# Optimization experiments

Hardware: AMD Instinct MI355X
Metric: run time of the kernel (lower is better)

## Reference

```python
import jax, jax.numpy as jnp
import numpy as np

H, W = 16, 16
DIM = 512
HEADS = 8
DIM_HEAD = 64
INNER = HEADS * DIM_HEAD  # 512
B = 8
N = H * W  # 256
SCALE = DIM_HEAD ** -0.5
EPS = 1e-5


def _index_map(h, w):
    # index_map[n, m] = dx * (2w-1) + dy with dx = x-i+h-1, dy = y-j+w-1
    xs = np.arange(h)
    ys = np.arange(w)
    dx = xs[:, None] - xs[None, :] + h - 1            # (h, h)
    dy = ys[:, None] - ys[None, :] + w - 1            # (w, w)
    idx = dx[:, None, :, None] * (2 * w - 1) + dy[None, :, None, :]  # (h, w, h, w)
    return idx.reshape(h * w, h * w).astype(np.int32)


def setup_inputs() -> dict:
    key = jax.random.key(0)
    ks = jax.random.split(key, 5)
    x = jax.random.normal(ks[0], (B, N, DIM), dtype=jnp.float32)
    ln_g = jnp.ones((DIM,), jnp.float32)
    ln_b = jnp.zeros((DIM,), jnp.float32)
    w_qkv = jax.random.normal(ks[1], (DIM, 3 * INNER), jnp.float32) * 0.02
    unique_params = jax.random.normal(ks[2], ((2 * H - 1) * (2 * W - 1), INNER), jnp.float32) * 0.02
    w_out = jax.random.normal(ks[3], (INNER, DIM), jnp.float32) * 0.02
    b_out = jnp.zeros((DIM,), jnp.float32)
    idx_map = jnp.asarray(_index_map(H, W))  # (N, N) int32
    return {"x": x, "ln_g": ln_g, "ln_b": ln_b, "w_qkv": w_qkv,
            "unique_params": unique_params, "w_out": w_out, "b_out": b_out,
            "idx_map": idx_map}


def reference(x, ln_g, ln_b, w_qkv, unique_params, w_out, b_out, idx_map):
    b, n, _ = x.shape
    # LayerNorm
    mu = jnp.mean(x, axis=-1, keepdims=True)
    var = jnp.mean(jnp.square(x - mu), axis=-1, keepdims=True)
    xn = (x - mu) * jax.lax.rsqrt(var + EPS) * ln_g + ln_b
    # qkv projection (no bias)
    qkv = xn @ w_qkv                                  # (b, n, 3*inner)
    q, k, v = jnp.split(qkv, 3, axis=-1)
    q = q.reshape(b, n, HEADS, DIM_HEAD)
    k = k.reshape(b, n, HEADS, DIM_HEAD)
    v = v.reshape(b, n, HEADS, DIM_HEAD)
    # attention scores
    dots = jnp.einsum('bnhd,bmhd->bhnm', q, k) * SCALE
    attn = jax.nn.softmax(dots, axis=-1)              # (b, h, n, m)
    # relative-position table: (n, m, h, d)
    rpos = unique_params[idx_map].reshape(n, n, HEADS, DIM_HEAD)
    # out[b,h,n,d] = sum_m attn[b,h,n,m] * (v[b,m,h,d] + rpos[n,m,h,d])
    out = jnp.einsum('bhnm,bmhd->bnhd', attn, v) \
        + jnp.einsum('bhnm,nmhd->bnhd', attn, rpos)
    out = out.reshape(b, n, INNER)
    return out @ w_out + b_out
```

## Files before the change

kernel.cpp:

```cpp
#include <hip/hip_runtime.h>
#include <math.h>

#define NB 8
#define SEQ 256
#define DIMC 512
#define NHEAD 8
#define DHEAD 64
#define SCALEF 0.125f

typedef __attribute__((ext_vector_type(8))) short s16x8;
typedef __attribute__((ext_vector_type(4))) float f32x4;

typedef __attribute__((address_space(3))) unsigned int lds_u32_t;
typedef const __attribute__((address_space(1))) unsigned int g_u32_t;
static __device__ __forceinline__ void gl_lds16(const void* gsrc, void* ldst) {
  __builtin_amdgcn_global_load_lds((g_u32_t*)gsrc, (lds_u32_t*)ldst, 16, 0, 0);
}

static __device__ __forceinline__ unsigned short f2bf(float f) {
  union { float f; unsigned u; } c; c.f = f;
  unsigned r = c.u + 0x7FFF + ((c.u >> 16) & 1);
  return (unsigned short)(r >> 16);
}

static __device__ void tcast_body(const float* __restrict__ W,
    unsigned short* __restrict__ WT, int K, int N, int n0, int k0, int t,
    float (*tile)[65]) {
#pragma unroll
  for (int i = 0; i < 16; ++i) {
    const int idx = i * 256 + t;
    const int kl = idx >> 6, nl = idx & 63;
    tile[kl][nl] = W[(size_t)(k0 + kl) * N + n0 + nl];
  }
  __syncthreads();
#pragma unroll
  for (int i = 0; i < 16; ++i) {
    const int idx = i * 256 + t;
    const int nl = idx >> 6, kl = idx & 63;
    WT[(size_t)(n0 + nl) * K + k0 + kl] = f2bf(tile[kl][nl]);
  }
}

__global__ __launch_bounds__(256) void prep_kernel(const float* __restrict__ x,
    const float* __restrict__ g, const float* __restrict__ bta,
    const float* __restrict__ w_qkv, const float* __restrict__ w_out,
    const float* __restrict__ up, unsigned short* __restrict__ xnb,
    unsigned short* __restrict__ wqt, unsigned short* __restrict__ wot,
    unsigned short* __restrict__ upT) {
  __shared__ float tile[64][65];
  __shared__ float sh_s[4], sh_q[4];
  const int t = threadIdx.x;
  const int bid = blockIdx.x;
  if (bid < 192) {
    tcast_body(w_qkv, wqt, 512, 1536, (bid % 24) * 64, (bid / 24) * 64, t, tile);
  } else if (bid < 256) {
    const int b2 = bid - 192;
    tcast_body(w_out, wot, 512, 512, (b2 % 8) * 64, (b2 / 8) * 64, t, tile);
  } else if (bid < 384) {
    const int b2 = bid - 256;
    const int k0 = (b2 >> 3) * 64, n0 = (b2 & 7) * 64;
#pragma unroll
    for (int i = 0; i < 16; ++i) {
      const int idx = i * 256 + t;
      const int kl = idx >> 6, nl = idx & 63;
      const int k = k0 + kl;
      tile[kl][nl] = (k < 961) ? up[(size_t)k * 512 + n0 + nl] : 0.0f;
    }
    __syncthreads();
#pragma unroll
    for (int i = 0; i < 16; ++i) {
      const int idx = i * 256 + t;
      const int nl = idx >> 6, kl = idx & 63;
      if (k0 + kl < 992)
        upT[(size_t)(n0 + nl) * 992 + k0 + kl] = f2bf(tile[kl][nl]);
    }
  } else {
    const int row = bid - 384;
    const float2 v = ((const float2*)(x + (size_t)row * DIMC))[t];
    float s = v.x + v.y;
    float q = v.x * v.x + v.y * v.y;
#pragma unroll
    for (int off = 32; off > 0; off >>= 1) {
      s += __shfl_down(s, off);
      q += __shfl_down(q, off);
    }
    const int wave = t >> 6, lane = t & 63;
    if (lane == 0) { sh_s[wave] = s; sh_q[wave] = q; }
    __syncthreads();
    const float fs = sh_s[0] + sh_s[1] + sh_s[2] + sh_s[3];
    const float fq = sh_q[0] + sh_q[1] + sh_q[2] + sh_q[3];
    const float mean = fs * (1.0f / DIMC);
    const float inv = rsqrtf(fq * (1.0f / DIMC) - mean * mean + 1e-5f);
    const float2 gv = ((const float2*)g)[t];
    const float2 bv = ((const float2*)bta)[t];
    ushort2 o;
    o.x = f2bf((v.x - mean) * inv * gv.x + bv.x);
    o.y = f2bf((v.y - mean) * inv * gv.y + bv.y);
    ((ushort2*)(xnb + (size_t)row * DIMC))[t] = o;
  }
}

template <int BM, int BN, bool BIAS, bool OUTBF, bool VSPLIT>
__global__ __launch_bounds__(256) void mfma_gemm_bt(
    const unsigned short* __restrict__ A, const unsigned short* __restrict__ BT,
    const float* __restrict__ bias, void* __restrict__ Cv,
    unsigned short* __restrict__ vtb, int M, int K, int N) {
  constexpr int TR = BM / 32;
  constexpr int TC = BN / 32;
  __shared__ unsigned short As[BM * 32];
  __shared__ unsigned short Bs[BN * 32];
  const int t = threadIdx.x;
  const int wave = t >> 6, lane = t & 63;
  const int wr = wave >> 1, wc = wave & 1;
  const int bm = blockIdx.x * BM, bn = blockIdx.y * BN;

  f32x4 acc[TR][TC] = {};

  const int fr = lane & 15, q4 = lane >> 4;
  const int kBlocks = K >> 5;
  for (int kb = 0; kb < kBlocks; ++kb) {
    const int k0 = kb << 5;
    __syncthreads();
#pragma unroll
    for (int c = 0; c < (BM * 4 + 255) / 256; ++c) {
      const int p = c * 256 + t;
      if (BM * 4 % 256 == 0 || p < BM * 4) {
        const int row = p >> 2;
        const int jl = (p & 3) ^ ((row >> 1) & 3);
        gl_lds16(A + (size_t)(bm + row) * K + k0 + jl * 8,
                 As + (size_t)(c * 256 + wave * 64) * 8);
      }
    }
#pragma unroll
    for (int c = 0; c < (BN * 4 + 255) / 256; ++c) {
      const int p = c * 256 + t;
      if (BN * 4 % 256 == 0 || p < BN * 4) {
        const int row = p >> 2;
        const int jl = (p & 3) ^ ((row >> 1) & 3);
        gl_lds16(BT + (size_t)(bn + row) * K + k0 + jl * 8,
                 Bs + (size_t)(c * 256 + wave * 64) * 8);
      }
    }
    __syncthreads();
    s16x8 af[TR], bfr[TC];
#pragma unroll
    for (int i = 0; i < TR; ++i) {
      const int row = wr * (BM / 2) + i * 16 + fr;
      const int jp = q4 ^ ((row >> 1) & 3);
      af[i] = *(const s16x8*)(As + row * 32 + jp * 8);
    }
#pragma unroll
    for (int j = 0; j < TC; ++j) {
      const int row = wc * (BN / 2) + j * 16 + fr;
      const int jp = q4 ^ ((row >> 1) & 3);
      bfr[j] = *(const s16x8*)(Bs + row * 32 + jp * 8);
    }
#pragma unroll
    for (int i = 0; i < TR; ++i)
#pragma unroll
      for (int j = 0; j < TC; ++j)
        acc[i][j] = __builtin_amdgcn_mfma_f32_16x16x32_bf16(af[i], bfr[j],
                                                            acc[i][j], 0, 0, 0);
  }
  if (VSPLIT && bn >= 1024) {
#pragma unroll
    for (int i = 0; i < TR; ++i) {
#pragma unroll
      for (int j = 0; j < TC; ++j) {
        const int hc = bn - 1024 + wc * (BN / 2) + j * 16 + fr;
        const int h = hc >> 6, d = hc & 63;
#pragma unroll
        for (int r = 0; r < 4; ++r) {
          const int row = bm + wr * (BM / 2) + i * 16 + q4 * 4 + r;
          const int b = row >> 8, m = row & 255;
          vtb[(size_t)((b * 8 + h) * 64 + d) * 256 + m] = f2bf(acc[i][j][r]);
        }
      }
    }
    return;
  }
#pragma unroll
  for (int i = 0; i < TR; ++i) {
#pragma unroll
    for (int j = 0; j < TC; ++j) {
      const int col = bn + wc * (BN / 2) + j * 16 + fr;
      const float bv = BIAS ? bias[col] : 0.0f;
#pragma unroll
      for (int r = 0; r < 4; ++r) {
        const int row = bm + wr * (BM / 2) + i * 16 + q4 * 4 + r;
        if constexpr (OUTBF) {
          ((unsigned short*)Cv)[(size_t)row * N + col] = f2bf(acc[i][j][r] + bv);
        } else {
          ((float*)Cv)[(size_t)row * N + col] = acc[i][j][r] + bv;
        }
      }
    }
  }
}

#define PSTR 264
#define ASTR2 520
__global__ __launch_bounds__(256) void attn_rpos_kernel(
    const unsigned short* __restrict__ qkvb,
    const unsigned short* __restrict__ vtb,
    const unsigned short* __restrict__ upT,
    unsigned short* __restrict__ ob) {
  __shared__ unsigned short ascat[16 * ASTR2];
  __shared__ unsigned short p_lds[16 * PSTR];
  __shared__ float smax[4][16], ssum[4][16];
  const int bh = blockIdx.y, b = bh >> 3, h = bh & 7;
  const int xn = blockIdx.x;
  const int n0 = xn * 16;
  const int t = threadIdx.x, wave = t >> 6, lane = t & 63;
  const int fr = lane & 15, q4 = lane >> 4;
  const int kwin0 = (xn * 31) & ~7;

  {
    const s16x8 z = {0, 0, 0, 0, 0, 0, 0, 0};
#pragma unroll
    for (int i = 0; i < 5; ++i) {
      const int idx = i * 256 + t;
      if (idx < 16 * ASTR2 / 8) *(s16x8*)(ascat + idx * 8) = z;
    }
  }

  s16x8 qf[2];
  {
    const size_t qrow = (size_t)(b * SEQ + n0 + fr) * 1536 + h * 64;
#pragma unroll
    for (int ks = 0; ks < 2; ++ks)
      qf[ks] = *(const s16x8*)(qkvb + qrow + ks * 32 + q4 * 8);
  }

  f32x4 s[4];
#pragma unroll
  for (int j = 0; j < 4; ++j) s[j] = (f32x4){0.f, 0.f, 0.f, 0.f};
  {
    const unsigned short* kb =
        qkvb + (size_t)(b * SEQ + wave * 64 + fr) * 1536 + 512 + h * 64;
#pragma unroll
    for (int ks = 0; ks < 2; ++ks)
#pragma unroll
      for (int j = 0; j < 4; ++j) {
        const s16x8 kf =
            *(const s16x8*)(kb + (size_t)j * (16 * 1536) + ks * 32 + q4 * 8);
        s[j] = __builtin_amdgcn_mfma_f32_16x16x32_bf16(qf[ks], kf, s[j], 0, 0, 0);
      }
  }

  float mx[4] = {-1e30f, -1e30f, -1e30f, -1e30f};
#pragma unroll
  for (int j = 0; j < 4; ++j)
#pragma unroll
    for (int r = 0; r < 4; ++r) {
      s[j][r] *= SCALEF;
      mx[r] = fmaxf(mx[r], s[j][r]);
    }
#pragma unroll
  for (int r = 0; r < 4; ++r) {
    mx[r] = fmaxf(mx[r], __shfl_xor(mx[r], 1));
    mx[r] = fmaxf(mx[r], __shfl_xor(mx[r], 2));
    mx[r] = fmaxf(mx[r], __shfl_xor(mx[r], 4));
    mx[r] = fmaxf(mx[r], __shfl_xor(mx[r], 8));
  }
  if (fr == 0) {
#pragma unroll
    for (int r = 0; r < 4; ++r) smax[wave][q4 * 4 + r] = mx[r];
  }
  __syncthreads();

  float fm[4];
#pragma unroll
  for (int r = 0; r < 4; ++r) {
    const int row = q4 * 4 + r;
    fm[r] = fmaxf(fmaxf(smax[0][row], smax[1][row]),
                  fmaxf(smax[2][row], smax[3][row]));
  }
  float sum[4] = {0.f, 0.f, 0.f, 0.f};
#pragma unroll
  for (int j = 0; j < 4; ++j)
#pragma unroll
    for (int r = 0; r < 4; ++r) {
      s[j][r] = __expf(s[j][r] - fm[r]);
      sum[r] += s[j][r];
    }
#pragma unroll
  for (int r = 0; r < 4; ++r) {
    sum[r] += __shfl_xor(sum[r], 1);
    sum[r] += __shfl_xor(sum[r], 2);
    sum[r] += __shfl_xor(sum[r], 4);
    sum[r] += __shfl_xor(sum[r], 8);
  }
  if (fr == 0) {
#pragma unroll
    for (int r = 0; r < 4; ++r) ssum[wave][q4 * 4 + r] = sum[r];
  }
  __syncthreads();

  float invs[4];
#pragma unroll
  for (int r = 0; r < 4; ++r) {
    const int row = q4 * 4 + r;
    invs[r] = 1.0f / (ssum[0][row] + ssum[1][row] + ssum[2][row] + ssum[3][row]);
  }

#pragma unroll
  for (int j = 0; j < 4; ++j) {
    const int mt = wave * 4 + j;
#pragma unroll
    for (int r = 0; r < 4; ++r) {
      const int row = q4 * 4 + r;
      const unsigned short pb = f2bf(s[j][r] * invs[r]);
      p_lds[row * PSTR + mt * 16 + fr] = pb;
      const int c = (xn - mt + 15) * 31 + (row - fr + 15) - kwin0;
      ascat[row * ASTR2 + c] = pb;
    }
  }
  __syncthreads();

  f32x4 oA = (f32x4){0.f, 0.f, 0.f, 0.f}, oB = oA, oC = oA, oD = oA;
  {
    const unsigned short* uB =
        upT + (size_t)(h * 64 + wave * 16 + fr) * 992 + kwin0;
    const unsigned short* aR = ascat + fr * ASTR2;
#pragma unroll
    for (int ks = 0; ks < 8; ++ks) {
      const s16x8 af = *(const s16x8*)(aR + ks * 32 + q4 * 8);
      const s16x8 bfg = *(const s16x8*)(uB + ks * 32 + q4 * 8);
      oA = __builtin_amdgcn_mfma_f32_16x16x32_bf16(af, bfg, oA, 0, 0, 0);
    }
#pragma unroll
    for (int ks = 8; ks < 16; ++ks) {
      const s16x8 af = *(const s16x8*)(aR + ks * 32 + q4 * 8);
      const s16x8 bfg = *(const s16x8*)(uB + ks * 32 + q4 * 8);
      oB = __builtin_amdgcn_mfma_f32_16x16x32_bf16(af, bfg, oB, 0, 0, 0);
    }
  }
  {
    const unsigned short* vB = vtb + (size_t)(bh * 64 + wave * 16 + fr) * 256;
    const unsigned short* pR = p_lds + fr * PSTR;
#pragma unroll
    for (int ks = 0; ks < 4; ++ks) {
      const s16x8 pf = *(const s16x8*)(pR + ks * 32 + q4 * 8);
      const s16x8 vfg = *(const s16x8*)(vB + ks * 32 + q4 * 8);
      oC = __builtin_amdgcn_mfma_f32_16x16x32_bf16(pf, vfg, oC, 0, 0, 0);
    }
#pragma unroll
    for (int ks = 4; ks < 8; ++ks) {
      const s16x8 pf = *(const s16x8*)(pR + ks * 32 + q4 * 8);
      const s16x8 vfg = *(const s16x8*)(vB + ks * 32 + q4 * 8);
      oD = __builtin_amdgcn_mfma_f32_16x16x32_bf16(pf, vfg, oD, 0, 0, 0);
    }
  }
  const f32x4 o = (oA + oB) + (oC + oD);
#pragma unroll
  for (int r = 0; r < 4; ++r) {
    const int n = n0 + q4 * 4 + r;
    ob[(size_t)(b * SEQ + n) * DIMC + h * 64 + wave * 16 + fr] = f2bf(o[r]);
  }
}

extern "C" void kernel_launch(void* const* d_in, const int* in_sizes, int n_in,
                              void* d_out, int out_size, void* d_ws,
                              size_t ws_size, hipStream_t stream) {
  const float* x = (const float*)d_in[0];
  const float* ln_g = (const float*)d_in[1];
  const float* ln_b = (const float*)d_in[2];
  const float* w_qkv = (const float*)d_in[3];
  const float* up = (const float*)d_in[4];
  const float* w_out = (const float*)d_in[5];
  const float* b_out = (const float*)d_in[6];
  float* out = (float*)d_out;

  unsigned short* u = (unsigned short*)d_ws;
  unsigned short* qkvb = u;
  unsigned short* xnb = u + 3145728;
  unsigned short* ob = u + 4194304;
  unsigned short* wqt = u + 5242880;
  unsigned short* wot = u + 6029312;
  unsigned short* upT = u + 6291456;
  unsigned short* vtb = u + 6799360;
  if (ws_size < (size_t)7847936 * sizeof(unsigned short)) return;

  prep_kernel<<<2432, 256, 0, stream>>>(x, ln_g, ln_b, w_qkv, w_out, up,
                                        xnb, wqt, wot, upT);
  mfma_gemm_bt<64, 64, false, true, true>
      <<<dim3(32, 24), 256, 0, stream>>>(xnb, wqt, nullptr, qkvb, vtb,
                                         2048, 512, 1536);
  attn_rpos_kernel<<<dim3(16, 64), 256, 0, stream>>>(qkvb, vtb, upT, ob);
  mfma_gemm_bt<64, 32, true, false, false>
      <<<dim3(32, 16), 256, 0, stream>>>(ob, wot, b_out, out, nullptr,
                                         2048, 512, 512);
}
```

Measured before the change: 111.3 us.

## Load GEMM fragments directly from global memory and add MFMA priority hints

The two projection GEMMs no longer stage A and B tiles through LDS with global_load_lds and barriers. Each wave now loads its MFMA fragments straight from global memory, with K fixed at compile time and the loop unrolled by four. The V-transpose epilogue packs four bf16 values into a single ushort4 store, and the attention kernel wraps its MFMA loops in s_setprio. This removes LDS traffic and block barriers, at the cost of redundant global and L2 reads across waves plus strided, less coalesced fragment loads.

```diff
diff --git a/kernel.cpp b/kernel.cpp
--- a/kernel.cpp
+++ b/kernel.cpp
@@ -1,21 +1,12 @@
 #include <hip/hip_runtime.h>
 #include <math.h>
 
-#define NB 8
 #define SEQ 256
 #define DIMC 512
-#define NHEAD 8
-#define DHEAD 64
 #define SCALEF 0.125f
 
 typedef __attribute__((ext_vector_type(8))) short s16x8;
 typedef __attribute__((ext_vector_type(4))) float f32x4;
-
-typedef __attribute__((address_space(3))) unsigned int lds_u32_t;
-typedef const __attribute__((address_space(1))) unsigned int g_u32_t;
-static __device__ __forceinline__ void gl_lds16(const void* gsrc, void* ldst) {
-  __builtin_amdgcn_global_load_lds((g_u32_t*)gsrc, (lds_u32_t*)ldst, 16, 0, 0);
-}
 
 static __device__ __forceinline__ unsigned short f2bf(float f) {
   union { float f; unsigned u; } c; c.f = f;
@@ -100,61 +91,32 @@
   }
 }
 
-template <int BM, int BN, bool BIAS, bool OUTBF, bool VSPLIT>
-__global__ __launch_bounds__(256) void mfma_gemm_bt(
+template <int BM, int BN, int K, bool BIAS, bool OUTBF, bool VSPLIT>
+__global__ __launch_bounds__(256) void gemm_direct(
     const unsigned short* __restrict__ A, const unsigned short* __restrict__ BT,
     const float* __restrict__ bias, void* __restrict__ Cv,
-    unsigned short* __restrict__ vtb, int M, int K, int N) {
+    unsigned short* __restrict__ vtb, int M, int N) {
   constexpr int TR = BM / 32;
   constexpr int TC = BN / 32;
-  __shared__ unsigned short As[BM * 32];
-  __shared__ unsigned short Bs[BN * 32];
   const int t = threadIdx.x;
   const int wave = t >> 6, lane = t & 63;
   const int wr = wave >> 1, wc = wave & 1;
+  const int fr = lane & 15, q4 = lane >> 4;
   const int bm = blockIdx.x * BM, bn = blockIdx.y * BN;
 
   f32x4 acc[TR][TC] = {};
-
-  const int fr = lane & 15, q4 = lane >> 4;
-  const int kBlocks = K >> 5;
-  for (int kb = 0; kb < kBlocks; ++kb) {
-    const int k0 = kb << 5;
-    __syncthreads();
-#pragma unroll
-    for (int c = 0; c < (BM * 4 + 255) / 256; ++c) {
-      const int p = c * 256 + t;
-      if (BM * 4 % 256 == 0 || p < BM * 4) {
-        const int row = p >> 2;
-        const int jl = (p & 3) ^ ((row >> 1) & 3);
-        gl_lds16(A + (size_t)(bm + row) * K + k0 + jl * 8,
-                 As + (size_t)(c * 256 + wave * 64) * 8);
-      }
-    }
-#pragma unroll
-    for (int c = 0; c < (BN * 4 + 255) / 256; ++c) {
-      const int p = c * 256 + t;
-      if (BN * 4 % 256 == 0 || p < BN * 4) {
-        const int row = p >> 2;
-        const int jl = (p & 3) ^ ((row >> 1) & 3);
-        gl_lds16(BT + (size_t)(bn + row) * K + k0 + jl * 8,
-                 Bs + (size_t)(c * 256 + wave * 64) * 8);
-      }
-    }
-    __syncthreads();
+  const unsigned short* Ap = A + (size_t)(bm + wr * (BM / 2) + fr) * K + q4 * 8;
+  const unsigned short* Bp = BT + (size_t)(bn + wc * (BN / 2) + fr) * K + q4 * 8;
+
+#pragma unroll 4
+  for (int k0 = 0; k0 < K; k0 += 32) {
     s16x8 af[TR], bfr[TC];
 #pragma unroll
-    for (int i = 0; i < TR; ++i) {
-      const int row = wr * (BM / 2) + i * 16 + fr;
-      const int jp = q4 ^ ((row >> 1) & 3);
-      af[i] = *(const s16x8*)(As + row * 32 + jp * 8);
-    }
-#pragma unroll
-    for (int j = 0; j < TC; ++j) {
-      const int row = wc * (BN / 2) + j * 16 + fr;
-      const int jp = q4 ^ ((row >> 1) & 3);
-      bfr[j] = *(const s16x8*)(Bs + row * 32 + jp * 8);
-    }
+    for (int i = 0; i < TR; ++i)
+      af[i] = *(const s16x8*)(Ap + (size_t)(i * 16) * K + k0);
+#pragma unroll
+    for (int j = 0; j < TC; ++j)
+      bfr[j] = *(const s16x8*)(Bp + (size_t)(j * 16) * K + k0);
 #pragma unroll
     for (int i = 0; i < TR; ++i)
 #pragma unroll
@@ -162,6 +124,7 @@
         acc[i][j] = __builtin_amdgcn_mfma_f32_16x16x32_bf16(af[i], bfr[j],
                                                             acc[i][j], 0, 0, 0);
   }
+
   if (VSPLIT && bn >= 1024) {
 #pragma unroll
     for (int i = 0; i < TR; ++i) {
@@ -169,12 +132,12 @@
       for (int j = 0; j < TC; ++j) {
         const int hc = bn - 1024 + wc * (BN / 2) + j * 16 + fr;
         const int h = hc >> 6, d = hc & 63;
-#pragma unroll
-        for (int r = 0; r < 4; ++r) {
-          const int row = bm + wr * (BM / 2) + i * 16 + q4 * 4 + r;
-          const int b = row >> 8, m = row & 255;
-          vtb[(size_t)((b * 8 + h) * 64 + d) * 256 + m] = f2bf(acc[i][j][r]);
-        }
+        const int row = bm + wr * (BM / 2) + i * 16 + q4 * 4;
+        const int b = row >> 8, m = row & 255;
+        ushort4 w;
+        w.x = f2bf(acc[i][j][0]); w.y = f2bf(acc[i][j][1]);
+        w.z = f2bf(acc[i][j][2]); w.w = f2bf(acc[i][j][3]);
+        *(ushort4*)&vtb[(size_t)((b * 8 + h) * 64 + d) * 256 + m] = w;
       }
     }
     return;
@@ -238,6 +201,7 @@
   {
     const unsigned short* kb =
         qkvb + (size_t)(b * SEQ + wave * 64 + fr) * 1536 + 512 + h * 64;
+    __builtin_amdgcn_s_setprio(1);
 #pragma unroll
     for (int ks = 0; ks < 2; ++ks)
 #pragma unroll
@@ -246,6 +210,7 @@
             *(const s16x8*)(kb + (size_t)j * (16 * 1536) + ks * 32 + q4 * 8);
         s[j] = __builtin_amdgcn_mfma_f32_16x16x32_bf16(qf[ks], kf, s[j], 0, 0, 0);
       }
+    __builtin_amdgcn_s_setprio(0);
   }
 
   float mx[4] = {-1e30f, -1e30f, -1e30f, -1e30f};
@@ -323,6 +288,7 @@
     const unsigned short* uB =
         upT + (size_t)(h * 64 + wave * 16 + fr) * 992 + kwin0;
     const unsigned short* aR = ascat + fr * ASTR2;
+    __builtin_amdgcn_s_setprio(1);
 #pragma unroll
     for (int ks = 0; ks < 8; ++ks) {
       const s16x8 af = *(const s16x8*)(aR + ks * 32 + q4 * 8);
@@ -335,10 +301,12 @@
       const s16x8 bfg = *(const s16x8*)(uB + ks * 32 + q4 * 8);
       oB = __builtin_amdgcn_mfma_f32_16x16x32_bf16(af, bfg, oB, 0, 0, 0);
     }
+    __builtin_amdgcn_s_setprio(0);
   }
   {
     const unsigned short* vB = vtb + (size_t)(bh * 64 + wave * 16 + fr) * 256;
     const unsigned short* pR = p_lds + fr * PSTR;
+    __builtin_amdgcn_s_setprio(1);
 #pragma unroll
     for (int ks = 0; ks < 4; ++ks) {
       const s16x8 pf = *(const s16x8*)(pR + ks * 32 + q4 * 8);
@@ -351,6 +319,7 @@
       const s16x8 vfg = *(const s16x8*)(vB + ks * 32 + q4 * 8);
       oD = __builtin_amdgcn_mfma_f32_16x16x32_bf16(pf, vfg, oD, 0, 0, 0);
     }
+    __builtin_amdgcn_s_setprio(0);
   }
   const f32x4 o = (oA + oB) + (oC + oD);
 #pragma unroll
@@ -384,11 +353,11 @@
 
   prep_kernel<<<2432, 256, 0, stream>>>(x, ln_g, ln_b, w_qkv, w_out, up,
                                         xnb, wqt, wot, upT);
-  mfma_gemm_bt<64, 64, false, true, true>
+  gemm_direct<64, 64, 512, false, true, true>
       <<<dim3(32, 24), 256, 0, stream>>>(xnb, wqt, nullptr, qkvb, vtb,
-                                         2048, 512, 1536);
+                                         2048, 1536);
   attn_rpos_kernel<<<dim3(16, 64), 256, 0, stream>>>(qkvb, vtb, upT, ob);
-  mfma_gemm_bt<64, 32, true, false, false>
+  gemm_direct<64, 32, 512, true, false, false>
       <<<dim3(32, 16), 256, 0, stream>>>(ob, wot, b_out, out, nullptr,
-                                         2048, 512, 512);
-}
+                                         2048, 512);
+}
```

New measurement: 129.5 us. 1.16x slower.
